# Kernel tuning notes

Hardware: AMD Instinct MI355X
Metric: run time of the kernel (lower is better)

Reference implementation:

```python
import jax, jax.numpy as jnp
import numpy as np
from jax import lax

N_KERNELS = 10000
KSS = np.array([7, 9, 11])
SEQ_LEN = 512
C_IN = 1
KMAX = 11  # max kernel size; shorter kernels are zero-padded in the tap dim
BATCH = 16


def _gen_params():
    # Deterministic ROCKET kernel hyperparameters (matches the torch __init__ logic).
    rng = np.random.default_rng(0)
    ks = rng.choice(KSS, size=N_KERNELS)
    hi = np.log2((SEQ_LEN - 1) // (ks - 1))
    dil = np.floor(2.0 ** rng.uniform(0.0, hi)).astype(np.int64)  # int(dilation)
    use_pad = rng.integers(0, 2, N_KERNELS)
    p = ((ks - 1) * dil // 2) * use_pad
    # Conv1d is called with padding=2*p (faithful to source), so output length is:
    L = SEQ_LEN + 4 * p - dil * (ks - 1)
    return ks, dil, p, L

_KS, _DIL, _P, _L = _gen_params()
_PMAX = int((2 * _P).max())   # max per-side zero padding across kernels
_LMAX = int(_L.max())         # max conv output length across kernels


def setup_inputs() -> dict:
    key = jax.random.key(0)
    kx, kw, kb = jax.random.split(key, 3)
    x = jax.random.normal(kx, (BATCH, C_IN, SEQ_LEN), dtype=jnp.float32)
    W = jax.random.normal(kw, (N_KERNELS, C_IN, KMAX), dtype=jnp.float32)
    # zero taps beyond each kernel's true size, then subtract mean over real taps
    tap_mask = jnp.asarray((np.arange(KMAX)[None, :] < _KS[:, None])[:, None, :],
                           dtype=jnp.float32)                      # [K,1,KMAX]
    denom = jnp.asarray((_KS * C_IN).astype(np.float32))[:, None, None]
    W = W * tap_mask
    W = (W - W.sum(axis=(1, 2), keepdims=True) / denom) * tap_mask
    bias = 2.0 * (jax.random.uniform(kb, (N_KERNELS,), dtype=jnp.float32) - 0.5)
    return {"x": x, "W": W, "bias": bias}


def reference(x, W, bias):
    B = x.shape[0]
    off = jnp.asarray(_PMAX - 2 * _P, dtype=jnp.int32)               # [K]
    dil = jnp.asarray(_DIL, dtype=jnp.int32)                         # [K]
    t = jnp.arange(_LMAX, dtype=jnp.int32)
    pos_base = off[:, None] + t[None, :]                             # [K, Lmax]
    valid = t[None, :] < jnp.asarray(_L, dtype=jnp.int32)[:, None]   # [K, Lmax]
    xpad = jnp.pad(x, ((0, 0), (0, 0), (_PMAX, _PMAX)))              # zero pad
    hi = SEQ_LEN + 2 * _PMAX - 1

    def step(acc, jw):
        j, wj = jw                                                   # wj: [K, C]
        pos = jnp.clip(pos_base + j * dil[:, None], 0, hi)           # [K, Lmax]
        xg = xpad[:, :, pos]                                         # [B,C,K,Lmax]
        return acc + jnp.einsum('bckl,kc->bkl', xg, wj), None

    acc0 = jnp.zeros((B, N_KERNELS, _LMAX), dtype=x.dtype)
    Wt = jnp.transpose(W, (2, 0, 1))                                 # [KMAX,K,C]
    acc, _ = lax.scan(step, acc0, (jnp.arange(KMAX, dtype=jnp.int32), Wt))
    out = acc + bias[None, :, None]                                  # [B,K,Lmax]

    # inputs are finite, so nGood == L (>0 always): max over valid region + PPV
    _max = jnp.where(valid[None], out, -jnp.inf).max(axis=-1)        # [B, K]
    ngood = jnp.asarray(_L, dtype=x.dtype)
    ppv = jnp.sum(jnp.where(valid[None], out > 0, False), axis=-1).astype(x.dtype) / ngood[None]
    return jnp.stack([_max, ppv], axis=-1).reshape(B, 2 * N_KERNELS)
```

## Files before the change

### kernel.cpp

```cpp
#include <hip/hip_runtime.h>
#include <hip/hip_fp16.h>
#include <math.h>
#include <stdint.h>
#include <string.h>

typedef unsigned __int128 u128;
typedef _Float16 h2v __attribute__((ext_vector_type(2)));
typedef short    s2v __attribute__((ext_vector_type(2)));

#define NK 10000
#define KPB 8

#define PCG_MUL_128 ((((u128)0x2360ed051fc65da4ULL) << 64) | 0x4385df649fccf645ULL)

#define SORT_OFF   (NK * 4)
#define WS_NEEDED  (SORT_OFF + NK * 4)

struct ThrTab { double t[3][84]; };

static void host_seed(u128& state, u128& inc) {
  uint32_t hc = 0x43b0d7e5u;
  auto hashmix = [&hc](uint32_t v) -> uint32_t {
    v ^= hc; hc *= 0x931e8875u; v *= hc; v ^= v >> 16; return v;
  };
  uint32_t pool[4];
  for (int i = 0; i < 4; ++i) pool[i] = hashmix(0u);
  for (int s = 0; s < 4; ++s)
    for (int d = 0; d < 4; ++d)
      if (s != d) {
        uint32_t h = hashmix(pool[s]);
        uint32_t r = pool[d] * 0xca01f9ddu - h * 0x4973f715u;
        r ^= r >> 16;
        pool[d] = r;
      }
  uint32_t hb = 0x8b51f9ddu;
  uint32_t w[8];
  for (int i = 0; i < 8; ++i) {
    uint32_t v = pool[i & 3];
    v ^= hb; hb *= 0x58f38dedu; v *= hb; v ^= v >> 16;
    w[i] = v;
  }
  u128 is_ = ((u128)(((uint64_t)w[0]) | ((uint64_t)w[1] << 32)) << 64)
           | (u128)(((uint64_t)w[2]) | ((uint64_t)w[3] << 32));
  u128 iq  = ((u128)(((uint64_t)w[4]) | ((uint64_t)w[5] << 32)) << 64)
           | (u128)(((uint64_t)w[6]) | ((uint64_t)w[7] << 32));
  inc = (iq << 1) | (u128)1;
  state = inc; state += is_; state = state * PCG_MUL_128 + inc;
}

static inline uint64_t xslrr_h(u128 s) {
  uint64_t x = (uint64_t)(s >> 64) ^ (uint64_t)s;
  unsigned r = (unsigned)(s >> 122);
  return (x >> r) | (x << ((64u - r) & 63u));
}

__device__ __forceinline__ void dev_seed(u128& state, u128& inc) {
  uint32_t hc = 0x43b0d7e5u;
  auto hashmix = [&hc](uint32_t v) -> uint32_t {
    v ^= hc; hc *= 0x931e8875u; v *= hc; v ^= v >> 16; return v;
  };
  uint32_t pool[4];
  for (int i = 0; i < 4; ++i) pool[i] = hashmix(0u);
  for (int s = 0; s < 4; ++s)
    for (int d = 0; d < 4; ++d)
      if (s != d) {
        uint32_t h = hashmix(pool[s]);
        uint32_t r = pool[d] * 0xca01f9ddu - h * 0x4973f715u;
        r ^= r >> 16;
        pool[d] = r;
      }
  uint32_t hb = 0x8b51f9ddu;
  uint32_t w[8];
  for (int i = 0; i < 8; ++i) {
    uint32_t v = pool[i & 3];
    v ^= hb; hb *= 0x58f38dedu; v *= hb; v ^= v >> 16;
    w[i] = v;
  }
  u128 is_ = ((u128)(((uint64_t)w[0]) | ((uint64_t)w[1] << 32)) << 64)
           | (u128)(((uint64_t)w[2]) | ((uint64_t)w[3] << 32));
  u128 iq  = ((u128)(((uint64_t)w[4]) | ((uint64_t)w[5] << 32)) << 64)
           | (u128)(((uint64_t)w[6]) | ((uint64_t)w[7] << 32));
  inc = (iq << 1) | (u128)1;
  state = inc; state += is_; state = state * PCG_MUL_128 + inc;
}

__device__ __forceinline__ u128 dev_advance(u128 state, u128 inc, uint64_t delta) {
  u128 am = 1, ap = 0, cm = PCG_MUL_128, cp = inc;
  while (delta) {
    if (delta & 1) { am = am * cm; ap = ap * cm + cp; }
    cp = (cm + (u128)1) * cp;
    cm = cm * cm;
    delta >>= 1;
  }
  return am * state + ap;
}

__device__ __forceinline__ uint64_t draw_at(u128 state, u128 inc, uint64_t n) {
  u128 s = dev_advance(state, inc, n);
  s = s * PCG_MUL_128 + inc;
  uint64_t x = (uint64_t)(s >> 64) ^ (uint64_t)s;
  unsigned r = (unsigned)(s >> 122);
  return (x >> r) | (x << ((64u - r) & 63u));
}

__global__ __launch_bounds__(256) void params_k(uint32_t* __restrict__ pack,
                                                ThrTab tt) {
  int i = blockIdx.x * 256 + threadIdx.x;
  if (i >= NK) return;
  u128 state, inc;
  dev_seed(state, inc);
  uint64_t a = draw_at(state, inc, (uint64_t)(i >> 1));
  uint32_t u = (i & 1) ? (uint32_t)(a >> 32) : (uint32_t)a;
  int si = (int)(((uint64_t)u * 3ull) >> 32);
  uint64_t ud = draw_at(state, inc, (uint64_t)(5000 + i));
  double d = (double)(ud >> 11) * (1.0 / 9007199254740992.0);
  int c0 = 0, c1 = 0, c2 = 0;
  #pragma unroll
  for (int v = 0; v < 84; ++v) {
    c0 += (d >= tt.t[0][v]) ? 1 : 0;
    c1 += (d >= tt.t[1][v]) ? 1 : 0;
    c2 += (d >= tt.t[2][v]) ? 1 : 0;
  }
  int dil = 1 + ((si == 0) ? c0 : ((si == 1) ? c1 : c2));
  uint64_t p6 = draw_at(state, inc, (uint64_t)(15000 + (i >> 1)));
  uint32_t pu = (i & 1) ? (uint32_t)(p6 >> 32) : (uint32_t)p6;
  int pad = (int)(pu >> 31);
  pack[i] = ((uint32_t)i << 10) | (uint32_t)si | ((uint32_t)dil << 2)
          | ((uint32_t)pad << 9);
}

__global__ __launch_bounds__(1024) void sort_k(const uint32_t* __restrict__ pack,
                                               uint32_t* __restrict__ sorted) {
  __shared__ int hist[1024];
  __shared__ int offs[1024];
  int tid = threadIdx.x;
  hist[tid] = 0;
  __syncthreads();
  for (int p = 0; p < 10; ++p) {
    int i = tid + p * 1024;
    if (i < NK) {
      uint32_t bits = pack[i] & 1023u;
      int ks = 7 + 2 * (int)(bits & 3), dil = (int)((bits >> 2) & 127);
      int pad = (int)(bits >> 9);
      int twop = (ks - 1) * dil * pad;
      int L = 512 + 2 * twop - dil * (ks - 1);
      atomicAdd(&hist[1022 - L], 1);
    }
  }
  __syncthreads();
  int own = hist[tid];
  for (int off = 1; off < 1024; off <<= 1) {
    int v = (tid >= off) ? hist[tid - off] : 0;
    __syncthreads();
    hist[tid] += v;
    __syncthreads();
  }
  offs[tid] = hist[tid] - own;
  __syncthreads();
  for (int p = 0; p < 10; ++p) {
    int i = tid + p * 1024;
    if (i < NK) {
      uint32_t e = pack[i];
      uint32_t bits = e & 1023u;
      int ks = 7 + 2 * (int)(bits & 3), dil = (int)((bits >> 2) & 127);
      int pad = (int)(bits >> 9);
      int twop = (ks - 1) * dil * pad;
      int L = 512 + 2 * twop - dil * (ks - 1);
      int idx = atomicAdd(&offs[1022 - L], 1);
      sorted[idx] = e;
    }
  }
}

template<int KS>
__device__ __forceinline__ void conv_core(const float4* __restrict__ xs4,
                                          const __half2* wh2, __half2 bvh2,
                                          int twop, int dil, int L,
                                          int tl, int bh,
                                          h2v* mh, s2v* ch) {
  const h2v zero2 = (h2v)0;
  int coreEnd = (L < 512) ? L : 512;
  int nch = (L + 31) >> 5;
  for (int c = 0; c < nch; ++c) {
    int t0 = c << 5;
    int t = t0 + tl;
    __half2 acc[4];
    #pragma unroll
    for (int r = 0; r < 4; ++r) acc[r] = bvh2;
    if (t0 >= twop && t0 + 32 <= coreEnd) {
      const float4* p = xs4 + (unsigned)(t - twop) * 2 + bh;
      #pragma unroll
      for (int j = 0; j < KS; ++j) {
        float4 v4 = *p;
        union { float4 v; __half2 h[4]; } u;
        u.v = v4;
        __half2 wj = wh2[j];
        #pragma unroll
        for (int r = 0; r < 4; ++r) acc[r] = __hfma2(wj, u.h[r], acc[r]);
        p += (unsigned)dil * 2;
      }
    } else {
      int idx = t - twop;
      #pragma unroll
      for (int j = 0; j < KS; ++j) {
        unsigned ci = (unsigned)idx;
        ci = (ci > 512u) ? 512u : ci;
        float4 v4 = xs4[ci * 2 + bh];
        union { float4 v; __half2 h[4]; } u;
        u.v = v4;
        __half2 wj = wh2[j];
        #pragma unroll
        for (int r = 0; r < 4; ++r) acc[r] = __hfma2(wj, u.h[r], acc[r]);
        idx += dil;
      }
    }
    if (t < L) {
      #pragma unroll
      for (int r = 0; r < 4; ++r) {
        union { __half2 h; h2v v; } cv;
        cv.h = acc[r];
        mh[r] = __builtin_elementwise_max(mh[r], cv.v);
        ch[r] -= (cv.v > zero2);
      }
    }
  }
}

__global__ __launch_bounds__(512) void conv_feat_k(const float* __restrict__ x,
                                                   const float* __restrict__ W,
                                                   const float* __restrict__ bias,
                                                   const uint32_t* __restrict__ entries,
                                                   float failDiag,
                                                   float* __restrict__ out) {
  __shared__ float4 xs4[513 * 2];
  int tid = threadIdx.x;

  #pragma unroll
  for (int q = 0; q < 2; ++q) {
    int flat = q * 512 + tid;
    int t = flat >> 1, bh = flat & 1;
    union { __half h[8]; float4 v; } u;
    #pragma unroll
    for (int r = 0; r < 8; ++r)
      u.h[r] = __float2half(x[(8 * bh + r) * 512 + t]);
    xs4[flat] = u.v;
  }
  if (tid < 2) xs4[512 * 2 + tid] = make_float4(0.f, 0.f, 0.f, 0.f);

  int wave = tid >> 6, lane = tid & 63;
  int tl = lane >> 1, bh = lane & 1;
  uint32_t e = entries[blockIdx.x * KPB + wave];
  int k = (int)(e >> 10);
  uint32_t bits = e & 1023u;
  __syncthreads();

  int ks  = 7 + 2 * (int)(bits & 3);
  int dil = (int)((bits >> 2) & 127);
  int pad = (int)(bits >> 9);
  int twop = (ks - 1) * dil * pad;
  int L = 512 + 2 * twop - dil * (ks - 1);
  float w10 = W[k * 11 + 10], w8 = W[k * 11 + 8];
  int ksW = (w10 != 0.0f) ? 11 : ((w8 != 0.0f) ? 9 : 7);
  if (failDiag != 0.0f || ks != ksW) {
    float diag = (failDiag != 0.0f) ? failDiag : 6500000.0f;
    if (lane < 16) {
      out[(size_t)lane * 20000 + 2 * k]     = diag;
      out[(size_t)lane * 20000 + 2 * k + 1] = diag;
    }
    return;
  }

  __half2 wh2[11];
  #pragma unroll
  for (int j = 0; j < 11; ++j) wh2[j] = __float2half2_rn(W[k * 11 + j]);
  __half2 bvh2 = __float2half2_rn(bias[k]);

  h2v mh[4];
  s2v ch[4];
  #pragma unroll
  for (int r = 0; r < 4; ++r) {
    mh[r] = (h2v)(-__builtin_huge_valf16());
    ch[r] = (s2v)0;
  }
  if (ks == 7)       conv_core<7>(xs4, wh2, bvh2, twop, dil, L, tl, bh, mh, ch);
  else if (ks == 9)  conv_core<9>(xs4, wh2, bvh2, twop, dil, L, tl, bh, mh, ch);
  else               conv_core<11>(xs4, wh2, bvh2, twop, dil, L, tl, bh, mh, ch);

  float m[8];
  int cn[8];
  #pragma unroll
  for (int r = 0; r < 4; ++r) {
    m[2 * r]      = (float)mh[r].x;
    m[2 * r + 1]  = (float)mh[r].y;
    cn[2 * r]     = (int)ch[r].x;
    cn[2 * r + 1] = (int)ch[r].y;
  }
  #pragma unroll
  for (int off = 2; off <= 32; off <<= 1) {
    #pragma unroll
    for (int r = 0; r < 8; ++r) {
      m[r] = fmaxf(m[r], __shfl_xor(m[r], off));
      cn[r] += __shfl_xor(cn[r], off);
    }
  }
  if (tl == 0) {
    float invL = 1.0f / (float)L;
    #pragma unroll
    for (int r = 0; r < 8; ++r) {
      size_t b = (size_t)(8 * bh + r);
      out[b * 20000 + 2 * k]     = m[r];
      out[b * 20000 + 2 * k + 1] = (float)cn[r] * invL;
    }
  }
}

extern "C" void kernel_launch(void* const* d_in, const int* in_sizes, int n_in,
                              void* d_out, int out_size, void* d_ws, size_t ws_size,
                              hipStream_t stream) {
  (void)out_size;
  const float *x = nullptr, *W = nullptr, *bias = nullptr;
  for (int i = 0; i < n_in; ++i) {
    int sz = in_sizes[i];
    if (sz == 16 * 512)      x    = (const float*)d_in[i];
    else if (sz == NK * 11)  W    = (const float*)d_in[i];
    else if (sz == NK)       bias = (const float*)d_in[i];
  }
  float failDiag = 0.0f;
  if (!x || !W || !bias) {
    failDiag = 9000000.0f;
    x = (const float*)d_in[0]; W = (const float*)d_in[1]; bias = (const float*)d_in[2];
  }

  static uint64_t hs[20000];
  {
    u128 st, inc; host_seed(st, inc);
    for (int i = 0; i < 20000; ++i) { st = st * PCG_MUL_128 + inc; hs[i] = xslrr_h(st); }
  }
  double d0 = (double)(hs[0] >> 11) * (1.0 / 9007199254740992.0);
  if (failDiag == 0.0f && fabs(d0 - 0.6369616873214543) >= 1.0e-15)
    failDiag = 4000000.0f;
  int rejected = 0;
  for (int i = 0; i < 5000; ++i)
    if ((uint32_t)hs[i] == 0u || (uint32_t)(hs[i] >> 32) == 0u) { rejected = 1; break; }

  static ThrTab tt;
  for (int si = 0; si < 3; ++si) {
    int ksv = 7 + 2 * si;
    double hi = log2((double)(511 / (ksv - 1)));
    double dmax = nextafter(1.0, 0.0);
    for (int v = 2; v <= 85; ++v) {
      if (pow(2.0, hi * dmax) < (double)v) { tt.t[si][v - 2] = 2.0; continue; }
      uint64_t lo = 0, hb;
      memcpy(&hb, &dmax, 8);
      while (hb - lo > 1) {
        uint64_t mid = lo + (hb - lo) / 2;
        double dm;
        memcpy(&dm, &mid, 8);
        if (pow(2.0, hi * dm) >= (double)v) hb = mid; else lo = mid;
      }
      double tv;
      memcpy(&tv, &hb, 8);
      tt.t[si][v - 2] = tv;
    }
  }

  uint32_t* dpack = (uint32_t*)d_ws;
  uint32_t* dsort = (uint32_t*)((char*)d_ws + SORT_OFF);

  if (!rejected && ws_size >= WS_NEEDED) {
    params_k<<<(NK + 255) / 256, 256, 0, stream>>>(dpack, tt);
    sort_k<<<1, 1024, 0, stream>>>(dpack, dsort);
    conv_feat_k<<<NK / KPB, 512, 0, stream>>>(x, W, bias, dsort, failDiag,
                                              (float*)d_out);
  } else {
    static uint32_t h_entries[NK];
    {
      int pos32 = 0;
      auto nx32 = [&](int& p) -> uint32_t {
        uint64_t v = hs[p >> 1];
        uint32_t u = (p & 1) ? (uint32_t)(v >> 32) : (uint32_t)v;
        ++p; return u;
      };
      static int ksA[NK], dilA[NK], padA[NK];
      for (int i = 0; i < NK; ++i) {
        uint64_t m; uint32_t u;
        do { u = nx32(pos32); m = (uint64_t)u * 3ull; } while ((uint32_t)m == 0u);
        ksA[i] = (int)(m >> 32);
      }
      int u64pos = (pos32 + 1) >> 1;
      for (int i = 0; i < NK; ++i) {
        double d = (double)(hs[u64pos + i] >> 11) * (1.0 / 9007199254740992.0);
        int ksv = 7 + 2 * ksA[i];
        double hi2 = log2((double)(511 / (ksv - 1)));
        dilA[i] = (int)floor(pow(2.0, hi2 * d));
      }
      int p32 = 2 * (u64pos + NK);
      for (int i = 0; i < NK; ++i) padA[i] = (int)(nx32(p32) >> 31);
      static int cnt2[1024], off2[1024];
      for (int b = 0; b < 1024; ++b) cnt2[b] = 0;
      for (int i = 0; i < NK; ++i) {
        int ksv = 7 + 2 * ksA[i];
        int twop = (ksv - 1) * dilA[i] * padA[i];
        int L = 512 + 2 * twop - dilA[i] * (ksv - 1);
        cnt2[1022 - L]++;
      }
      int acc = 0;
      for (int b = 0; b < 1024; ++b) { off2[b] = acc; acc += cnt2[b]; }
      for (int i = 0; i < NK; ++i) {
        int ksv = 7 + 2 * ksA[i];
        int twop = (ksv - 1) * dilA[i] * padA[i];
        int L = 512 + 2 * twop - dilA[i] * (ksv - 1);
        uint32_t bits = (uint32_t)ksA[i] | ((uint32_t)dilA[i] << 2)
                      | ((uint32_t)padA[i] << 9);
        h_entries[off2[1022 - L]++] = ((uint32_t)i << 10) | bits;
      }
    }
    (void)hipMemcpyAsync(dsort, h_entries, sizeof(h_entries),
                         hipMemcpyHostToDevice, stream);
    conv_feat_k<<<NK / KPB, 512, 0, stream>>>(x, W, bias, dsort, failDiag,
                                              (float*)d_out);
  }
}
```

Baseline: 71.79 us.

## Fuse parameter generation with per-block bucket sort and drop separate sort kernel

The separate single-block sort kernel is removed. Each 256-thread params block now builds a shared-memory histogram of its own entries by output length, scans it, and writes them back sorted in place. This saves one kernel launch and the serial 1024-thread global sort. In exchange, kernels are only sorted by length within each 256-entry chunk rather than globally, which could weaken length grouping and load balance in the conv kernel.

```diff
diff --git a/kernel.cpp b/kernel.cpp
--- a/kernel.cpp
+++ b/kernel.cpp
@@ -13,8 +13,7 @@
 
 #define PCG_MUL_128 ((((u128)0x2360ed051fc65da4ULL) << 64) | 0x4385df649fccf645ULL)
 
-#define SORT_OFF   (NK * 4)
-#define WS_NEEDED  (SORT_OFF + NK * 4)
+#define WS_NEEDED  (NK * 4)
 
 struct ThrTab { double t[3][84]; };
 
@@ -105,70 +104,67 @@
 
 __global__ __launch_bounds__(256) void params_k(uint32_t* __restrict__ pack,
                                                 ThrTab tt) {
-  int i = blockIdx.x * 256 + threadIdx.x;
-  if (i >= NK) return;
-  u128 state, inc;
-  dev_seed(state, inc);
-  uint64_t a = draw_at(state, inc, (uint64_t)(i >> 1));
-  uint32_t u = (i & 1) ? (uint32_t)(a >> 32) : (uint32_t)a;
-  int si = (int)(((uint64_t)u * 3ull) >> 32);
-  uint64_t ud = draw_at(state, inc, (uint64_t)(5000 + i));
-  double d = (double)(ud >> 11) * (1.0 / 9007199254740992.0);
-  int c0 = 0, c1 = 0, c2 = 0;
-  #pragma unroll
-  for (int v = 0; v < 84; ++v) {
-    c0 += (d >= tt.t[0][v]) ? 1 : 0;
-    c1 += (d >= tt.t[1][v]) ? 1 : 0;
-    c2 += (d >= tt.t[2][v]) ? 1 : 0;
-  }
-  int dil = 1 + ((si == 0) ? c0 : ((si == 1) ? c1 : c2));
-  uint64_t p6 = draw_at(state, inc, (uint64_t)(15000 + (i >> 1)));
-  uint32_t pu = (i & 1) ? (uint32_t)(p6 >> 32) : (uint32_t)p6;
-  int pad = (int)(pu >> 31);
-  pack[i] = ((uint32_t)i << 10) | (uint32_t)si | ((uint32_t)dil << 2)
-          | ((uint32_t)pad << 9);
-}
-
-__global__ __launch_bounds__(1024) void sort_k(const uint32_t* __restrict__ pack,
-                                               uint32_t* __restrict__ sorted) {
   __shared__ int hist[1024];
+  __shared__ int scanbuf[256];
   __shared__ int offs[1024];
   int tid = threadIdx.x;
-  hist[tid] = 0;
+  int base = blockIdx.x * 256;
+  int n = NK - base; if (n > 256) n = 256;
+
+  uint32_t e = 0;
+  int bkt = -1;
+  if (tid < n) {
+    int i = base + tid;
+    u128 state, inc;
+    dev_seed(state, inc);
+    uint64_t a = draw_at(state, inc, (uint64_t)(i >> 1));
+    uint32_t u = (i & 1) ? (uint32_t)(a >> 32) : (uint32_t)a;
+    int si = (int)(((uint64_t)u * 3ull) >> 32);
+    uint64_t ud = draw_at(state, inc, (uint64_t)(5000 + i));
+    double d = (double)(ud >> 11) * (1.0 / 9007199254740992.0);
+    int c0 = 0, c1 = 0, c2 = 0;
+    #pragma unroll
+    for (int v = 0; v < 84; ++v) {
+      c0 += (d >= tt.t[0][v]) ? 1 : 0;
+      c1 += (d >= tt.t[1][v]) ? 1 : 0;
+      c2 += (d >= tt.t[2][v]) ? 1 : 0;
+    }
+    int dil = 1 + ((si == 0) ? c0 : ((si == 1) ? c1 : c2));
+    uint64_t p6 = draw_at(state, inc, (uint64_t)(15000 + (i >> 1)));
+    uint32_t pu = (i & 1) ? (uint32_t)(p6 >> 32) : (uint32_t)p6;
+    int pad = (int)(pu >> 31);
+    int ks = 7 + 2 * si;
+    int twop = (ks - 1) * dil * pad;
+    int L = 512 + 2 * twop - dil * (ks - 1);
+    e = ((uint32_t)i << 10) | (uint32_t)si | ((uint32_t)dil << 2)
+      | ((uint32_t)pad << 9);
+    bkt = 1022 - L;
+  }
+  #pragma unroll
+  for (int q = 0; q < 4; ++q) hist[tid + 256 * q] = 0;
   __syncthreads();
-  for (int p = 0; p < 10; ++p) {
-    int i = tid + p * 1024;
-    if (i < NK) {
-      uint32_t bits = pack[i] & 1023u;
-      int ks = 7 + 2 * (int)(bits & 3), dil = (int)((bits >> 2) & 127);
-      int pad = (int)(bits >> 9);
-      int twop = (ks - 1) * dil * pad;
-      int L = 512 + 2 * twop - dil * (ks - 1);
-      atomicAdd(&hist[1022 - L], 1);
-    }
-  }
+  if (bkt >= 0) atomicAdd(&hist[bkt], 1);
   __syncthreads();
-  int own = hist[tid];
-  for (int off = 1; off < 1024; off <<= 1) {
-    int v = (tid >= off) ? hist[tid - off] : 0;
+  int h0 = hist[4 * tid], h1 = hist[4 * tid + 1];
+  int h2 = hist[4 * tid + 2], h3 = hist[4 * tid + 3];
+  int s = h0 + h1 + h2 + h3;
+  scanbuf[tid] = s;
+  __syncthreads();
+  for (int off = 1; off < 256; off <<= 1) {
+    int v = (tid >= off) ? scanbuf[tid - off] : 0;
     __syncthreads();
-    hist[tid] += v;
+    scanbuf[tid] += v;
     __syncthreads();
   }
-  offs[tid] = hist[tid] - own;
+  int ex = scanbuf[tid] - s;
+  offs[4 * tid]     = ex;
+  offs[4 * tid + 1] = ex + h0;
+  offs[4 * tid + 2] = ex + h0 + h1;
+  offs[4 * tid + 3] = ex + h0 + h1 + h2;
   __syncthreads();
-  for (int p = 0; p < 10; ++p) {
-    int i = tid + p * 1024;
-    if (i < NK) {
-      uint32_t e = pack[i];
-      uint32_t bits = e & 1023u;
-      int ks = 7 + 2 * (int)(bits & 3), dil = (int)((bits >> 2) & 127);
-      int pad = (int)(bits >> 9);
-      int twop = (ks - 1) * dil * pad;
-      int L = 512 + 2 * twop - dil * (ks - 1);
-      int idx = atomicAdd(&offs[1022 - L], 1);
-      sorted[idx] = e;
-    }
+  if (bkt >= 0) {
+    int idx = atomicAdd(&offs[bkt], 1);
+    pack[base + idx] = e;
   }
 }
 
@@ -365,12 +361,10 @@
   }
 
   uint32_t* dpack = (uint32_t*)d_ws;
-  uint32_t* dsort = (uint32_t*)((char*)d_ws + SORT_OFF);
 
   if (!rejected && ws_size >= WS_NEEDED) {
     params_k<<<(NK + 255) / 256, 256, 0, stream>>>(dpack, tt);
-    sort_k<<<1, 1024, 0, stream>>>(dpack, dsort);
-    conv_feat_k<<<NK / KPB, 512, 0, stream>>>(x, W, bias, dsort, failDiag,
+    conv_feat_k<<<NK / KPB, 512, 0, stream>>>(x, W, bias, dpack, failDiag,
                                               (float*)d_out);
   } else {
     static uint32_t h_entries[NK];
@@ -415,9 +409,9 @@
         h_entries[off2[1022 - L]++] = ((uint32_t)i << 10) | bits;
       }
     }
-    (void)hipMemcpyAsync(dsort, h_entries, sizeof(h_entries),
+    (void)hipMemcpyAsync(dpack, h_entries, sizeof(h_entries),
                          hipMemcpyHostToDevice, stream);
-    conv_feat_k<<<NK / KPB, 512, 0, stream>>>(x, W, bias, dsort, failDiag,
+    conv_feat_k<<<NK / KPB, 512, 0, stream>>>(x, W, bias, dpack, failDiag,
                                               (float*)d_out);
   }
 }
```

Measured after the change: 95.35 us. 32.8% more time.
